# Kernel optimization log

Measured on AMD Instinct MI355X. Metric: run time of the kernel, lower is better.

The kernel has to match this reference:

```python
import jax, jax.numpy as jnp
import numpy as np

B, N, C, K, OUT = 4, 16384, 64, 16, 128
BN_EPS = 1e-5


def setup_inputs() -> dict:
    key = jax.random.key(0)
    ks = jax.random.split(key, 6)
    feature = jax.random.normal(ks[0], (B, C, N), dtype=jnp.float32)
    neigh_index = jax.random.randint(ks[1], (B * N, K), 0, B * N)
    permatrix = jnp.zeros((1,), dtype=jnp.float32)  # unused by forward
    # Conv1d(in_c, in_c, kernel_size=1, bias=False) -> weight [C, C]
    W_mlp = jax.random.normal(ks[2], (C, C), dtype=jnp.float32) / np.sqrt(C).astype(np.float32)
    # Linear(in_c, out_c) -> weight [OUT, C], bias [OUT]
    W_conv = jax.random.normal(ks[3], (OUT, C), dtype=jnp.float32) / np.sqrt(C).astype(np.float32)
    b_conv = jax.random.normal(ks[4], (OUT,), dtype=jnp.float32) * 0.01
    gamma = jnp.ones((OUT,), dtype=jnp.float32)
    beta = jnp.zeros((OUT,), dtype=jnp.float32)
    return {
        "feature": feature,
        "neigh_index": neigh_index,
        "permatrix": permatrix,
        "W_mlp": W_mlp,
        "W_conv": W_conv,
        "b_conv": b_conv,
        "gamma": gamma,
        "beta": beta,
    }


def reference(feature, neigh_index, permatrix, W_mlp, W_conv, b_conv, gamma, beta):
    bsize, feats, num_pts = feature.shape
    # [B, C, N] -> [B*N, C]
    flat = feature.transpose(0, 2, 1).reshape(bsize * num_pts, feats)
    # irregular gather: [B*N, k, C]
    spirals = flat[neigh_index]
    # 1x1 conv over channels: einsum with mlp weight [C_out=C, C_in=C]
    scores = jnp.einsum("nkc,dc->nkd", spirals, W_mlp)  # [B*N, k, C]
    # softmax over channel dim (torch dim=1 on [BN, C, k] layout)
    attn = jax.nn.softmax(scores, axis=-1)
    # attention pooling over the k neighbors -> [B*N, C]
    pooled = jnp.sum(attn * spirals, axis=1)
    # Linear: [B*N, OUT]
    out = pooled @ W_conv.T + b_conv
    # [B, OUT, N]
    out = out.reshape(bsize, num_pts, -1).transpose(0, 2, 1)
    # BatchNorm1d (training-mode batch statistics) over (batch, points) per channel
    mean = jnp.mean(out, axis=(0, 2), keepdims=True)
    var = jnp.var(out, axis=(0, 2), keepdims=True)
    out = (out - mean) * jax.lax.rsqrt(var + BN_EPS)
    out = out * gamma[None, :, None] + beta[None, :, None]
    return out
```

## Files before the change

### kernel.cpp

```cpp
#include <hip/hip_runtime.h>
#include <cstdint>

#define NPTS   16384
#define BATCH  4
#define BNP    65536
#define CIN    64
#define KNB    16
#define COUT   128
#define BN_EPS 1e-5f

typedef __attribute__((ext_vector_type(8))) short     short8;
typedef __attribute__((ext_vector_type(4))) float     f32x4;
typedef __attribute__((ext_vector_type(2))) unsigned  u32x2;
typedef __attribute__((ext_vector_type(4))) int       i32x4;

#define WAITVM(n) __builtin_amdgcn_s_waitcnt(0x0F70 | (n))

__device__ __forceinline__ unsigned short f2bf(float f) {
    unsigned u = __float_as_uint(f);
    u += 0x7FFFu + ((u >> 16) & 1u);
    return (unsigned short)(u >> 16);
}
__device__ __forceinline__ float bf2f(unsigned short h) {
    return __uint_as_float(((unsigned)h) << 16);
}

__global__ __launch_bounds__(256) void k_prep(const float* __restrict__ feat,
                                              unsigned short* __restrict__ fb)
{
    __shared__ float t[CIN][CIN + 1];
    int blk = blockIdx.x;
    int b   = blk >> 8;
    int n0  = (blk & 255) << 6;
    int sub = threadIdx.x >> 6, lane = threadIdx.x & 63;
    const float* fp = feat + (size_t)b * CIN * NPTS;
    #pragma unroll
    for (int r = 0; r < CIN; r += 4) {
        int c = r + sub;
        t[c][lane] = fp[(size_t)c * NPTS + n0 + lane];
    }
    __syncthreads();
    unsigned short* ob = fb + (size_t)(b * NPTS + n0) * CIN;
    #pragma unroll
    for (int r = 0; r < CIN; r += 4) {
        int x = r + sub;
        ob[(size_t)x * CIN + lane] = f2bf(t[lane][x]);
    }
}

__global__ __launch_bounds__(256, 2) void k_main(
    const unsigned short* __restrict__ fb,
    const int* __restrict__ nidx,
    const float* __restrict__ Wm,
    const float* __restrict__ Wc,
    float* __restrict__ out)
{
    __shared__ __align__(16) unsigned short spir[4][4][1024];
    __shared__ __align__(16) unsigned short plds[4][16 * 72];
    __shared__ __align__(16) int            idxl[4][16 * 20];

    const int tid  = threadIdx.x;
    const int wv   = tid >> 6;
    const int lane = tid & 63;
    const int ptc  = lane & 15;
    const int qg   = lane >> 4;
    const int pt4  = lane >> 2;
    const int q4   = lane & 3;

    short8 wmF[4][2];
    #pragma unroll
    for (int mt = 0; mt < 4; ++mt)
        #pragma unroll
        for (int ks = 0; ks < 2; ++ks) {
            const float* p = Wm + (size_t)(mt * 16 + ptc) * CIN + qg * 8 + ks * 32;
            short8 v;
            #pragma unroll
            for (int j = 0; j < 8; ++j) v[j] = (short)f2bf(p[j]);
            wmF[mt][ks] = v;
        }
    short8 wcF[8][2];
    #pragma unroll
    for (int mt = 0; mt < 8; ++mt)
        #pragma unroll
        for (int ks = 0; ks < 2; ++ks) {
            const float* p = Wc + (size_t)(mt * 16 + ptc) * CIN + qg * 8 + ks * 32;
            short8 v;
            #pragma unroll
            for (int j = 0; j < 8; ++j) v[j] = (short)f2bf(p[j]);
            wcF[mt][ks] = v;
        }

    for (int g = blockIdx.x * 4 + wv; g < BNP / KNB; g += 2048) {
        i32x4 iv = *(const i32x4*)(nidx + (size_t)g * 256 + lane * 4);
        *(i32x4*)&idxl[wv][pt4 * 20 + q4 * 4] = iv;

        auto issue_gather = [&](int k, int bf) {
            int id = idxl[wv][pt4 * 20 + k];
            const unsigned short* gp = fb + (size_t)id * CIN + q4 * 8;
            __builtin_amdgcn_global_load_lds(
                (const __attribute__((address_space(1))) unsigned int*)(const void*)gp,
                (__attribute__((address_space(3))) unsigned int*)(void*)&spir[wv][bf][0],
                16, 0, 0);
            __builtin_amdgcn_global_load_lds(
                (const __attribute__((address_space(1))) unsigned int*)(const void*)(gp + 32),
                (__attribute__((address_space(3))) unsigned int*)(void*)&spir[wv][bf][512],
                16, 0, 0);
        };

        issue_gather(0, 0);
        issue_gather(1, 1);
        issue_gather(2, 2);

        f32x4 pool[4];
        #pragma unroll
        for (int i = 0; i < 4; ++i) pool[i] = (f32x4){0.f, 0.f, 0.f, 0.f};

        #pragma unroll
        for (int k = 0; k < KNB; ++k) {
            const int bf = k & 3;
            if (k + 3 < KNB) issue_gather(k + 3, (k + 3) & 3);
            if      (k <= KNB - 4) WAITVM(6);
            else if (k == KNB - 3) WAITVM(4);
            else if (k == KNB - 2) WAITVM(2);
            else                   WAITVM(0);
            __asm__ volatile("" ::: "memory");

            short8 b1_0 = *(const short8*)&spir[wv][bf][      ptc * 32 + qg * 8];
            short8 b1_1 = *(const short8*)&spir[wv][bf][512 + ptc * 32 + qg * 8];
            f32x4 zero4 = (f32x4){0.f, 0.f, 0.f, 0.f};
            f32x4 a1[4];
            #pragma unroll
            for (int mt = 0; mt < 4; ++mt) {
                f32x4 t0 = __builtin_amdgcn_mfma_f32_16x16x32_bf16(wmF[mt][0], b1_0, zero4, 0, 0, 0);
                a1[mt]   = __builtin_amdgcn_mfma_f32_16x16x32_bf16(wmF[mt][1], b1_1, t0,    0, 0, 0);
            }

            float e[16], s = 0.f;
            #pragma unroll
            for (int mt = 0; mt < 4; ++mt)
                #pragma unroll
                for (int r = 0; r < 4; ++r) {
                    float x = __expf(a1[mt][r]);
                    e[mt * 4 + r] = x;
                    s += x;
                }
            s += __shfl_xor(s, 16);
            s += __shfl_xor(s, 32);
            float inv = __builtin_amdgcn_rcpf(s);

            #pragma unroll
            for (int mt = 0; mt < 4; ++mt) {
                u32x2 sv = *(const u32x2*)&spir[wv][bf]
                    [(mt >> 1) * 512 + ptc * 32 + (mt & 1) * 16 + qg * 4];
                unsigned lo = sv[0], hi = sv[1];
                pool[mt][0] = fmaf(bf2f((unsigned short)lo),         e[mt * 4 + 0] * inv, pool[mt][0]);
                pool[mt][1] = fmaf(bf2f((unsigned short)(lo >> 16)), e[mt * 4 + 1] * inv, pool[mt][1]);
                pool[mt][2] = fmaf(bf2f((unsigned short)hi),         e[mt * 4 + 2] * inv, pool[mt][2]);
                pool[mt][3] = fmaf(bf2f((unsigned short)(hi >> 16)), e[mt * 4 + 3] * inv, pool[mt][3]);
            }
        }

        #pragma unroll
        for (int mt = 0; mt < 4; ++mt) {
            unsigned w0 = ((__float_as_uint(pool[mt][0]) + 0x8000u) >> 16) |
                          ((__float_as_uint(pool[mt][1]) + 0x8000u) & 0xFFFF0000u);
            unsigned w1 = ((__float_as_uint(pool[mt][2]) + 0x8000u) >> 16) |
                          ((__float_as_uint(pool[mt][3]) + 0x8000u) & 0xFFFF0000u);
            *(u32x2*)&plds[wv][ptc * 72 + mt * 16 + qg * 4] = (u32x2){w0, w1};
        }
        short8 b2_0 = *(const short8*)&plds[wv][ptc * 72 +      qg * 8];
        short8 b2_1 = *(const short8*)&plds[wv][ptc * 72 + 32 + qg * 8];

        f32x4 acc2[8];
        #pragma unroll
        for (int mt = 0; mt < 8; ++mt) {
            f32x4 t0 = __builtin_amdgcn_mfma_f32_16x16x32_bf16(wcF[mt][0], b2_0,
                                                               (f32x4){0.f,0.f,0.f,0.f}, 0, 0, 0);
            acc2[mt] = __builtin_amdgcn_mfma_f32_16x16x32_bf16(wcF[mt][1], b2_1, t0, 0, 0, 0);
        }

        int p0 = g * KNB;
        int b  = p0 >> 14;
        int nn = (p0 & (NPTS - 1)) + ptc;
        float* ob = out + (((size_t)b * COUT) << 14) + nn;
        #pragma unroll
        for (int mt = 0; mt < 8; ++mt)
            #pragma unroll
            for (int r = 0; r < 4; ++r)
                ob[((size_t)(mt * 16 + qg * 4 + r)) << 14] = acc2[mt][r];
    }
}

__global__ __launch_bounds__(256) void k_part(const float* __restrict__ out,
                                              float* __restrict__ part)
{
    int o = blockIdx.x >> 2, b = blockIdx.x & 3;
    const float4* p = (const float4*)(out + (((size_t)(b * COUT + o)) << 14));
    float s = 0.f, q = 0.f;
    for (int i = threadIdx.x; i < NPTS / 4; i += 256) {
        float4 v = p[i];
        s += (v.x + v.y) + (v.z + v.w);
        q += (v.x * v.x + v.y * v.y) + (v.z * v.z + v.w * v.w);
    }
    #pragma unroll
    for (int off = 32; off >= 1; off >>= 1) {
        s += __shfl_xor(s, off);
        q += __shfl_xor(q, off);
    }
    __shared__ float ls[4], lq[4];
    if ((threadIdx.x & 63) == 0) { ls[threadIdx.x >> 6] = s; lq[threadIdx.x >> 6] = q; }
    __syncthreads();
    if (threadIdx.x == 0) {
        part[blockIdx.x * 2]     = (ls[0] + ls[1]) + (ls[2] + ls[3]);
        part[blockIdx.x * 2 + 1] = (lq[0] + lq[1]) + (lq[2] + lq[3]);
    }
}

__global__ __launch_bounds__(256) void k_apply(float* __restrict__ out,
                                               const float* __restrict__ part,
                                               const float* __restrict__ gamma,
                                               const float* __restrict__ beta)
{
    __shared__ float sc[COUT], sh[COUT];
    int t = threadIdx.x;
    if (t < COUT) {
        float s = 0.f, q = 0.f;
        #pragma unroll
        for (int j = 0; j < 4; ++j) {
            s += part[(t * 4 + j) * 2];
            q += part[(t * 4 + j) * 2 + 1];
        }
        float mean = s * (1.0f / BNP);
        float var  = q * (1.0f / BNP) - mean * mean;
        float a = gamma[t] * rsqrtf(var + BN_EPS);
        sc[t] = a; sh[t] = beta[t] - mean * a;
    }
    __syncthreads();
    const int total4 = BATCH * COUT * NPTS / 4;
    for (long i = (long)blockIdx.x * 256 + t; i < total4; i += (long)gridDim.x * 256) {
        int ch = ((int)(i >> 12)) & 127;
        float4 v = ((float4*)out)[i];
        float a = sc[ch], b2 = sh[ch];
        v.x = fmaf(v.x, a, b2); v.y = fmaf(v.y, a, b2);
        v.z = fmaf(v.z, a, b2); v.w = fmaf(v.w, a, b2);
        ((float4*)out)[i] = v;
    }
}

extern "C" void kernel_launch(void* const* d_in, const int* in_sizes, int n_in,
                              void* d_out, int out_size, void* d_ws, size_t ws_size,
                              hipStream_t stream)
{
    const float* feat  = (const float*)d_in[0];
    const int*   nidx  = (const int*)  d_in[1];
    const float* Wm    = (const float*)d_in[3];
    const float* Wc    = (const float*)d_in[4];
    const float* gamma = (const float*)d_in[6];
    const float* beta  = (const float*)d_in[7];
    float* out = (float*)d_out;

    unsigned short* fb = (unsigned short*)d_ws;
    float* part = (float*)((char*)d_ws + (size_t)BNP * CIN * 2);

    k_prep <<<1024, 256, 0, stream>>>(feat, fb);
    k_main <<<512,  256, 0, stream>>>(fb, nidx, Wm, Wc, out);
    k_part <<<512,  256, 0, stream>>>(out, part);
    k_apply<<<2048, 256, 0, stream>>>(out, part, gamma, beta);
}
```

Before: 181.3 us.

## Fuse BatchNorm statistics into main kernel with coalesced LDS-staged output stores

The separate per-channel statistics pass is removed. The main kernel now reduces sum and sum-of-squares in-block and adds them to a global accumulator with atomics, and an extra block in the prep kernel zeroes that accumulator. Output tiles are staged through swizzled LDS so each block writes contiguous float4 rows instead of strided scalar stores. The grid becomes one group per wave with occupancy hint 4, neighbour indices are shuffled from registers, and Wc is converted inside the loop to save registers. This avoids a full re-read of the output, at the cost of atomic contention and float-order nondeterminism.

```diff
diff --git a/kernel.cpp b/kernel.cpp
--- a/kernel.cpp
+++ b/kernel.cpp
@@ -26,8 +26,13 @@
 }
 
 __global__ __launch_bounds__(256) void k_prep(const float* __restrict__ feat,
-                                              unsigned short* __restrict__ fb)
-{
+                                              unsigned short* __restrict__ fb,
+                                              float* __restrict__ stat)
+{
+    if (blockIdx.x == 1024) {
+        stat[threadIdx.x] = 0.f;
+        return;
+    }
     __shared__ float t[CIN][CIN + 1];
     int blk = blockIdx.x;
     int b   = blk >> 8;
@@ -48,24 +53,24 @@
     }
 }
 
-__global__ __launch_bounds__(256, 2) void k_main(
+__global__ __launch_bounds__(256, 4) void k_main(
     const unsigned short* __restrict__ fb,
     const int* __restrict__ nidx,
     const float* __restrict__ Wm,
     const float* __restrict__ Wc,
-    float* __restrict__ out)
+    float* __restrict__ out,
+    float* __restrict__ stat)
 {
     __shared__ __align__(16) unsigned short spir[4][4][1024];
-    __shared__ __align__(16) unsigned short plds[4][16 * 72];
-    __shared__ __align__(16) int            idxl[4][16 * 20];
 
     const int tid  = threadIdx.x;
     const int wv   = tid >> 6;
     const int lane = tid & 63;
     const int ptc  = lane & 15;
     const int qg   = lane >> 4;
-    const int pt4  = lane >> 2;
     const int q4   = lane & 3;
+
+    const int g = blockIdx.x * 4 + wv;
 
     short8 wmF[4][2];
     #pragma unroll
@@ -78,160 +83,156 @@
             for (int j = 0; j < 8; ++j) v[j] = (short)f2bf(p[j]);
             wmF[mt][ks] = v;
         }
-    short8 wcF[8][2];
+
+    i32x4 iv = *(const i32x4*)(nidx + (size_t)g * 256 + lane * 4);
+
+    auto issue_gather = [&](int k, int bf) {
+        int id = __shfl(iv[k & 3], (lane & 0x3C) | (k >> 2));
+        const unsigned short* gp = fb + (size_t)id * CIN + q4 * 8;
+        __builtin_amdgcn_global_load_lds(
+            (const __attribute__((address_space(1))) unsigned int*)(const void*)gp,
+            (__attribute__((address_space(3))) unsigned int*)(void*)&spir[wv][bf][0],
+            16, 0, 0);
+        __builtin_amdgcn_global_load_lds(
+            (const __attribute__((address_space(1))) unsigned int*)(const void*)(gp + 32),
+            (__attribute__((address_space(3))) unsigned int*)(void*)&spir[wv][bf][512],
+            16, 0, 0);
+    };
+
+    issue_gather(0, 0);
+    issue_gather(1, 1);
+    issue_gather(2, 2);
+
+    f32x4 pool[4];
+    #pragma unroll
+    for (int i = 0; i < 4; ++i) pool[i] = (f32x4){0.f, 0.f, 0.f, 0.f};
+
+    #pragma unroll
+    for (int k = 0; k < KNB; ++k) {
+        const int bf = k & 3;
+        if (k + 3 < KNB) issue_gather(k + 3, (k + 3) & 3);
+        if      (k <= KNB - 4) WAITVM(6);
+        else if (k == KNB - 3) WAITVM(4);
+        else if (k == KNB - 2) WAITVM(2);
+        else                   WAITVM(0);
+        __asm__ volatile("" ::: "memory");
+
+        short8 b1_0 = *(const short8*)&spir[wv][bf][      ptc * 32 + qg * 8];
+        short8 b1_1 = *(const short8*)&spir[wv][bf][512 + ptc * 32 + qg * 8];
+        f32x4 zero4 = (f32x4){0.f, 0.f, 0.f, 0.f};
+        f32x4 a1[4];
+        #pragma unroll
+        for (int mt = 0; mt < 4; ++mt) {
+            f32x4 t0 = __builtin_amdgcn_mfma_f32_16x16x32_bf16(wmF[mt][0], b1_0, zero4, 0, 0, 0);
+            a1[mt]   = __builtin_amdgcn_mfma_f32_16x16x32_bf16(wmF[mt][1], b1_1, t0,    0, 0, 0);
+        }
+
+        float e[16], s = 0.f;
+        #pragma unroll
+        for (int mt = 0; mt < 4; ++mt)
+            #pragma unroll
+            for (int r = 0; r < 4; ++r) {
+                float x = __expf(a1[mt][r]);
+                e[mt * 4 + r] = x;
+                s += x;
+            }
+        s += __shfl_xor(s, 16);
+        s += __shfl_xor(s, 32);
+        float inv = __builtin_amdgcn_rcpf(s);
+
+        #pragma unroll
+        for (int mt = 0; mt < 4; ++mt) {
+            u32x2 sv = *(const u32x2*)&spir[wv][bf]
+                [(mt >> 1) * 512 + ptc * 32 + (mt & 1) * 16 + qg * 4];
+            unsigned lo = sv[0], hi = sv[1];
+            pool[mt][0] = fmaf(bf2f((unsigned short)lo),         e[mt * 4 + 0] * inv, pool[mt][0]);
+            pool[mt][1] = fmaf(bf2f((unsigned short)(lo >> 16)), e[mt * 4 + 1] * inv, pool[mt][1]);
+            pool[mt][2] = fmaf(bf2f((unsigned short)hi),         e[mt * 4 + 2] * inv, pool[mt][2]);
+            pool[mt][3] = fmaf(bf2f((unsigned short)(hi >> 16)), e[mt * 4 + 3] * inv, pool[mt][3]);
+        }
+    }
+
+    unsigned short* pl = &spir[wv][0][0];
+    #pragma unroll
+    for (int mt = 0; mt < 4; ++mt) {
+        unsigned w0 = ((__float_as_uint(pool[mt][0]) + 0x8000u) >> 16) |
+                      ((__float_as_uint(pool[mt][1]) + 0x8000u) & 0xFFFF0000u);
+        unsigned w1 = ((__float_as_uint(pool[mt][2]) + 0x8000u) >> 16) |
+                      ((__float_as_uint(pool[mt][3]) + 0x8000u) & 0xFFFF0000u);
+        *(u32x2*)&pl[ptc * 72 + mt * 16 + qg * 4] = (u32x2){w0, w1};
+    }
+    short8 b2_0 = *(const short8*)&pl[ptc * 72 +      qg * 8];
+    short8 b2_1 = *(const short8*)&pl[ptc * 72 + 32 + qg * 8];
+
+    f32x4 acc2[8];
+    #pragma unroll
+    for (int mt = 0; mt < 8; ++mt) {
+        const float* p = Wc + (size_t)(mt * 16 + ptc) * CIN + qg * 8;
+        short8 w0, w1;
+        #pragma unroll
+        for (int j = 0; j < 8; ++j) {
+            w0[j] = (short)f2bf(p[j]);
+            w1[j] = (short)f2bf(p[j + 32]);
+        }
+        f32x4 t0 = __builtin_amdgcn_mfma_f32_16x16x32_bf16(w0, b2_0,
+                                                           (f32x4){0.f,0.f,0.f,0.f}, 0, 0, 0);
+        acc2[mt] = __builtin_amdgcn_mfma_f32_16x16x32_bf16(w1, b2_1, t0, 0, 0, 0);
+    }
+
+    __syncthreads();
+    float* st = (float*)&spir[0][0][0];
     #pragma unroll
     for (int mt = 0; mt < 8; ++mt)
         #pragma unroll
-        for (int ks = 0; ks < 2; ++ks) {
-            const float* p = Wc + (size_t)(mt * 16 + ptc) * CIN + qg * 8 + ks * 32;
-            short8 v;
-            #pragma unroll
-            for (int j = 0; j < 8; ++j) v[j] = (short)f2bf(p[j]);
-            wcF[mt][ks] = v;
-        }
-
-    for (int g = blockIdx.x * 4 + wv; g < BNP / KNB; g += 2048) {
-        i32x4 iv = *(const i32x4*)(nidx + (size_t)g * 256 + lane * 4);
-        *(i32x4*)&idxl[wv][pt4 * 20 + q4 * 4] = iv;
-
-        auto issue_gather = [&](int k, int bf) {
-            int id = idxl[wv][pt4 * 20 + k];
-            const unsigned short* gp = fb + (size_t)id * CIN + q4 * 8;
-            __builtin_amdgcn_global_load_lds(
-                (const __attribute__((address_space(1))) unsigned int*)(const void*)gp,
-                (__attribute__((address_space(3))) unsigned int*)(void*)&spir[wv][bf][0],
-                16, 0, 0);
-            __builtin_amdgcn_global_load_lds(
-                (const __attribute__((address_space(1))) unsigned int*)(const void*)(gp + 32),
-                (__attribute__((address_space(3))) unsigned int*)(void*)&spir[wv][bf][512],
-                16, 0, 0);
-        };
-
-        issue_gather(0, 0);
-        issue_gather(1, 1);
-        issue_gather(2, 2);
-
-        f32x4 pool[4];
-        #pragma unroll
-        for (int i = 0; i < 4; ++i) pool[i] = (f32x4){0.f, 0.f, 0.f, 0.f};
-
-        #pragma unroll
-        for (int k = 0; k < KNB; ++k) {
-            const int bf = k & 3;
-            if (k + 3 < KNB) issue_gather(k + 3, (k + 3) & 3);
-            if      (k <= KNB - 4) WAITVM(6);
-            else if (k == KNB - 3) WAITVM(4);
-            else if (k == KNB - 2) WAITVM(2);
-            else                   WAITVM(0);
-            __asm__ volatile("" ::: "memory");
-
-            short8 b1_0 = *(const short8*)&spir[wv][bf][      ptc * 32 + qg * 8];
-            short8 b1_1 = *(const short8*)&spir[wv][bf][512 + ptc * 32 + qg * 8];
-            f32x4 zero4 = (f32x4){0.f, 0.f, 0.f, 0.f};
-            f32x4 a1[4];
-            #pragma unroll
-            for (int mt = 0; mt < 4; ++mt) {
-                f32x4 t0 = __builtin_amdgcn_mfma_f32_16x16x32_bf16(wmF[mt][0], b1_0, zero4, 0, 0, 0);
-                a1[mt]   = __builtin_amdgcn_mfma_f32_16x16x32_bf16(wmF[mt][1], b1_1, t0,    0, 0, 0);
-            }
-
-            float e[16], s = 0.f;
-            #pragma unroll
-            for (int mt = 0; mt < 4; ++mt)
-                #pragma unroll
-                for (int r = 0; r < 4; ++r) {
-                    float x = __expf(a1[mt][r]);
-                    e[mt * 4 + r] = x;
-                    s += x;
-                }
-            s += __shfl_xor(s, 16);
-            s += __shfl_xor(s, 32);
-            float inv = __builtin_amdgcn_rcpf(s);
-
-            #pragma unroll
-            for (int mt = 0; mt < 4; ++mt) {
-                u32x2 sv = *(const u32x2*)&spir[wv][bf]
-                    [(mt >> 1) * 512 + ptc * 32 + (mt & 1) * 16 + qg * 4];
-                unsigned lo = sv[0], hi = sv[1];
-                pool[mt][0] = fmaf(bf2f((unsigned short)lo),         e[mt * 4 + 0] * inv, pool[mt][0]);
-                pool[mt][1] = fmaf(bf2f((unsigned short)(lo >> 16)), e[mt * 4 + 1] * inv, pool[mt][1]);
-                pool[mt][2] = fmaf(bf2f((unsigned short)hi),         e[mt * 4 + 2] * inv, pool[mt][2]);
-                pool[mt][3] = fmaf(bf2f((unsigned short)(hi >> 16)), e[mt * 4 + 3] * inv, pool[mt][3]);
-            }
-        }
-
-        #pragma unroll
-        for (int mt = 0; mt < 4; ++mt) {
-            unsigned w0 = ((__float_as_uint(pool[mt][0]) + 0x8000u) >> 16) |
-                          ((__float_as_uint(pool[mt][1]) + 0x8000u) & 0xFFFF0000u);
-            unsigned w1 = ((__float_as_uint(pool[mt][2]) + 0x8000u) >> 16) |
-                          ((__float_as_uint(pool[mt][3]) + 0x8000u) & 0xFFFF0000u);
-            *(u32x2*)&plds[wv][ptc * 72 + mt * 16 + qg * 4] = (u32x2){w0, w1};
-        }
-        short8 b2_0 = *(const short8*)&plds[wv][ptc * 72 +      qg * 8];
-        short8 b2_1 = *(const short8*)&plds[wv][ptc * 72 + 32 + qg * 8];
-
-        f32x4 acc2[8];
-        #pragma unroll
-        for (int mt = 0; mt < 8; ++mt) {
-            f32x4 t0 = __builtin_amdgcn_mfma_f32_16x16x32_bf16(wcF[mt][0], b2_0,
-                                                               (f32x4){0.f,0.f,0.f,0.f}, 0, 0, 0);
-            acc2[mt] = __builtin_amdgcn_mfma_f32_16x16x32_bf16(wcF[mt][1], b2_1, t0, 0, 0, 0);
-        }
-
-        int p0 = g * KNB;
-        int b  = p0 >> 14;
-        int nn = (p0 & (NPTS - 1)) + ptc;
-        float* ob = out + (((size_t)b * COUT) << 14) + nn;
-        #pragma unroll
-        for (int mt = 0; mt < 8; ++mt)
-            #pragma unroll
-            for (int r = 0; r < 4; ++r)
-                ob[((size_t)(mt * 16 + qg * 4 + r)) << 14] = acc2[mt][r];
-    }
-}
-
-__global__ __launch_bounds__(256) void k_part(const float* __restrict__ out,
-                                              float* __restrict__ part)
-{
-    int o = blockIdx.x >> 2, b = blockIdx.x & 3;
-    const float4* p = (const float4*)(out + (((size_t)(b * COUT + o)) << 14));
-    float s = 0.f, q = 0.f;
-    for (int i = threadIdx.x; i < NPTS / 4; i += 256) {
-        float4 v = p[i];
-        s += (v.x + v.y) + (v.z + v.w);
-        q += (v.x * v.x + v.y * v.y) + (v.z * v.z + v.w * v.w);
-    }
-    #pragma unroll
-    for (int off = 32; off >= 1; off >>= 1) {
-        s += __shfl_xor(s, off);
-        q += __shfl_xor(q, off);
-    }
-    __shared__ float ls[4], lq[4];
-    if ((threadIdx.x & 63) == 0) { ls[threadIdx.x >> 6] = s; lq[threadIdx.x >> 6] = q; }
-    __syncthreads();
-    if (threadIdx.x == 0) {
-        part[blockIdx.x * 2]     = (ls[0] + ls[1]) + (ls[2] + ls[3]);
-        part[blockIdx.x * 2 + 1] = (lq[0] + lq[1]) + (lq[2] + lq[3]);
+        for (int r = 0; r < 4; ++r) {
+            int ch = mt * 16 + qg * 4 + r;
+            int f  = (wv * 16 + ptc) ^ ((ch & 7) << 2);
+            st[ch * 64 + f] = acc2[mt][r];
+        }
+    __syncthreads();
+
+    const int b  = blockIdx.x >> 8;
+    const int n0 = (blockIdx.x * 64) & (NPTS - 1);
+    float s_acc[8], q_acc[8];
+    #pragma unroll
+    for (int i = 0; i < 8; ++i) {
+        int flat = i * 256 + tid;
+        int ch   = flat >> 4;
+        int slot = flat & 15;
+        int f0   = (slot * 4) ^ ((ch & 7) << 2);
+        f32x4 v  = *(const f32x4*)&st[ch * 64 + f0];
+        *(f32x4*)(out + (((size_t)(b * COUT + ch)) << 14) + n0 + slot * 4) = v;
+        s_acc[i] = (v[0] + v[1]) + (v[2] + v[3]);
+        q_acc[i] = (v[0]*v[0] + v[1]*v[1]) + (v[2]*v[2] + v[3]*v[3]);
+    }
+    #pragma unroll
+    for (int m = 1; m <= 8; m <<= 1)
+        #pragma unroll
+        for (int i = 0; i < 8; ++i) {
+            s_acc[i] += __shfl_xor(s_acc[i], m);
+            q_acc[i] += __shfl_xor(q_acc[i], m);
+        }
+    if ((tid & 15) == 0) {
+        #pragma unroll
+        for (int i = 0; i < 8; ++i) {
+            int ch = i * 16 + (tid >> 4);
+            atomicAdd(&stat[ch],        s_acc[i]);
+            atomicAdd(&stat[COUT + ch], q_acc[i]);
+        }
     }
 }
 
 __global__ __launch_bounds__(256) void k_apply(float* __restrict__ out,
-                                               const float* __restrict__ part,
+                                               const float* __restrict__ stat,
                                                const float* __restrict__ gamma,
                                                const float* __restrict__ beta)
 {
     __shared__ float sc[COUT], sh[COUT];
     int t = threadIdx.x;
     if (t < COUT) {
-        float s = 0.f, q = 0.f;
-        #pragma unroll
-        for (int j = 0; j < 4; ++j) {
-            s += part[(t * 4 + j) * 2];
-            q += part[(t * 4 + j) * 2 + 1];
-        }
-        float mean = s * (1.0f / BNP);
-        float var  = q * (1.0f / BNP) - mean * mean;
+        float S = stat[t], Q = stat[COUT + t];
+        float mean = S * (1.0f / BNP);
+        float var  = Q * (1.0f / BNP) - mean * mean;
         float a = gamma[t] * rsqrtf(var + BN_EPS);
         sc[t] = a; sh[t] = beta[t] - mean * a;
     }
@@ -260,10 +261,9 @@
     float* out = (float*)d_out;
 
     unsigned short* fb = (unsigned short*)d_ws;
-    float* part = (float*)((char*)d_ws + (size_t)BNP * CIN * 2);
-
-    k_prep <<<1024, 256, 0, stream>>>(feat, fb);
-    k_main <<<512,  256, 0, stream>>>(fb, nidx, Wm, Wc, out);
-    k_part <<<512,  256, 0, stream>>>(out, part);
-    k_apply<<<2048, 256, 0, stream>>>(out, part, gamma, beta);
-}
+    float* stat = (float*)((char*)d_ws + (size_t)BNP * CIN * 2);
+
+    k_prep <<<1025, 256, 0, stream>>>(feat, fb, stat);
+    k_main <<<1024, 256, 0, stream>>>(fb, nidx, Wm, Wc, out, stat);
+    k_apply<<<2048, 256, 0, stream>>>(out, stat, gamma, beta);
+}
```

Result: slower. 302.5 us (+66.8%).
